# Optimization experiments

Measured on AMD Instinct MI355X. Metric: run time of the kernel, lower is better.

Reference implementation:

```python
import jax, jax.numpy as jnp
import numpy as np

K_PERIODS = 6


def setup_inputs() -> dict:
    key = jax.random.key(0)
    x = jax.random.normal(key, (16, 2048, 128), dtype=jnp.float32)
    return {"x": x}


def reference(x):
    # x: [B, T, N] -> out: [B, K, Pmax, N].
    # Pmax is data-dependent in the torch original (max selected period); here we
    # use the static upper bound Pmax = T so shapes are jit-static. Columns
    # p >= P_row are zero, matching the original's zero padding.
    B, T, N = x.shape
    BN = B * N
    seqs = jnp.transpose(x, (0, 2, 1)).reshape(BN, T)  # [BN, T]

    # --- top-k nonzero frequencies by spectral energy ---
    spec = jnp.fft.rfft(seqs, axis=-1)
    mag2 = spec.real ** 2 + spec.imag ** 2
    mag2 = mag2.at[:, 0].set(0.0)  # kill DC bin
    k = min(K_PERIODS, mag2.shape[-1] - 1)
    _, kidx = jax.lax.top_k(mag2, k)          # [BN, K]
    kidx = jnp.maximum(kidx, 1)

    # --- per-(row, freq) period geometry ---
    P = jnp.maximum(T // kidx, 1)             # [BN, K] period length
    cycles = jnp.maximum(T // P, 1)           # [BN, K] number of full cycles
    take = cycles * P
    base = jnp.maximum(T - take, 0)           # [BN, K] start offset

    # --- fold-and-average via scatter-add (no [BN,K,Cmax,Pmax] blowup) ---
    # element at time t >= base maps to phase p = (t - base) % P, averaged over cycles
    t = jnp.arange(T, dtype=jnp.int32)
    rel = t[None, None, :] - base[:, :, None]          # [BN, K, T]
    valid = rel >= 0
    p = jnp.where(valid, rel % P[:, :, None], 0)       # phase index in [0, P)
    vals = jnp.where(valid, seqs[:, None, :], 0.0)     # [BN, K, T]

    row = jnp.arange(BN * k, dtype=jnp.int32).reshape(BN, k, 1)
    seg_ids = row * T + p                               # flat segment id
    sums = jax.ops.segment_sum(vals.reshape(-1), seg_ids.reshape(-1),
                               num_segments=BN * k * T)
    seg = sums.reshape(BN, k, T) / cycles[:, :, None].astype(vals.dtype)

    out = seg.reshape(B, N, k, T).transpose(0, 2, 3, 1)  # [B, K, Pmax=T, N]
    return out
```

## Files before the change

### kernel.cpp

```cpp
#include <hip/hip_runtime.h>
#include <stdint.h>

#define TB   256
#define TLEN 2048
#define NB   16
#define NCH  128
#define BN   (NB*NCH)
#define KP   6

typedef unsigned long long u64;

__global__ __launch_bounds__(256) void k_fill0(float4* __restrict__ out, int n4) {
  int i = blockIdx.x * blockDim.x + threadIdx.x;
  int stride = gridDim.x * blockDim.x;
  float4 z = make_float4(0.f, 0.f, 0.f, 0.f);
  for (; i < n4; i += stride) out[i] = z;
}

__global__ __launch_bounds__(256) void k_transpose_in(const float* __restrict__ x,
                                                      float* __restrict__ seqs) {
  __shared__ float tile[64][65];
  int t0 = blockIdx.x * 64, n0 = blockIdx.y * 64, b = blockIdx.z;
  int tx = threadIdx.x & 63, ty = threadIdx.x >> 6;
#pragma unroll
  for (int tt = ty; tt < 64; tt += 4)
    tile[tt][tx] = x[(size_t)(b * TLEN + t0 + tt) * NCH + n0 + tx];
  __syncthreads();
#pragma unroll
  for (int nn = ty; nn < 64; nn += 4)
    seqs[(size_t)(b * NCH + n0 + nn) * TLEN + t0 + tx] = tile[tx][nn];
}

#define FT 512
__global__ __launch_bounds__(FT) void k_fft_topk(const float* __restrict__ seqs,
                                                 int4* __restrict__ params) {
  __shared__ float2 bufA[2048];
  __shared__ float2 bufB[2048];
  __shared__ float2 tw[1024];
  __shared__ u64 wmax[FT / 64];
  int tid = threadIdx.x;
  int r0 = blockIdx.x * 2;

  for (int t = tid; t < TLEN; t += FT) {
    float vr = seqs[(size_t)r0 * TLEN + t];
    float vi = seqs[(size_t)(r0 + 1) * TLEN + t];
    bufA[t] = make_float2(vr, vi);
  }
  const float c0 = -6.283185307179586f / 2048.0f;
  for (int j = tid; j < 1024; j += FT) {
    float sn, cs;
    sincosf(c0 * (float)j, &sn, &cs);
    tw[j] = make_float2(cs, sn);
  }

  float2* xb = bufA;
  float2* yb = bufB;
  for (int st = 0; st < 11; st++) {
    __syncthreads();
    int s = 1 << st;
#pragma unroll
    for (int ii = 0; ii < 1024 / FT; ii++) {
      int i = tid + ii * FT;
      int q = i & (s - 1);
      int p = i >> st;
      float2 a = xb[i];
      float2 b = xb[i + 1024];
      float2 w = tw[p << st];
      int o = q + (p << (st + 1));
      yb[o] = make_float2(a.x + b.x, a.y + b.y);
      float dx = a.x - b.x, dy = a.y - b.y;
      yb[o + s] = make_float2(dx * w.x - dy * w.y, dx * w.y + dy * w.x);
    }
    float2* t2 = xb; xb = yb; yb = t2;
  }
  __syncthreads();
  const float2* Z = xb;
  u64* keys = (u64*)bufA;
  for (int i = tid; i < 1024; i += FT) {
    int kb = i + 1;
    float2 zk = Z[kb];
    float2 zc = Z[2048 - kb];
    float ax = zk.x + zc.x, ay = zk.y - zc.y;
    float bx = zk.x - zc.x, by = zk.y + zc.y;
    float m2a = ax * ax + ay * ay;
    float m2b = bx * bx + by * by;
    keys[i]        = ((u64)__float_as_uint(m2a) << 32) | (unsigned)(0xFFFFFFFFu - (unsigned)kb);
    keys[1024 + i] = ((u64)__float_as_uint(m2b) << 32) | (unsigned)(0xFFFFFFFFu - (unsigned)kb);
  }
  __syncthreads();

  for (int rw = 0; rw < 2; rw++) {
    u64* kbase = keys + rw * 1024;
    for (int r = 0; r < KP; r++) {
      u64 best = 0ull;
      for (int i = tid; i < 1024; i += FT) {
        u64 v = kbase[i];
        best = v > best ? v : best;
      }
      for (int off = 32; off > 0; off >>= 1) {
        u64 o = __shfl_down(best, off);
        best = o > best ? o : best;
      }
      if ((tid & 63) == 0) wmax[tid >> 6] = best;
      __syncthreads();
      if (tid == 0) {
        best = wmax[0];
        for (int w = 1; w < FT / 64; w++) best = wmax[w] > best ? wmax[w] : best;
        int bin = (int)(0xFFFFFFFFu - (unsigned)(best & 0xFFFFFFFFull));
        if (bin < 1 || bin > 1024) bin = 1;
        kbase[bin - 1] = 0ull;
        int P = TLEN / bin;
        int cyc = TLEN / P;
        int base = TLEN - cyc * P;
        params[(r0 + rw) * KP + r] = make_int4(P, base, cyc, 0);
      }
      __syncthreads();
    }
  }
}

__global__ __launch_bounds__(256) void k_fold_row(const float* __restrict__ seqs,
                                                  const int4* __restrict__ params,
                                                  float* __restrict__ out) {
  __shared__ float srow[TLEN];
  __shared__ float acc[64];
  int row = blockIdx.x;
  int b = row >> 7, n = row & 127;
  int tid = threadIdx.x, lane = tid & 63, wv = tid >> 6;

  const float4* s4 = (const float4*)(seqs + (size_t)row * TLEN);
  float4* r4 = (float4*)srow;
  for (int i = tid; i < TLEN / 4; i += TB) r4[i] = s4[i];
  __syncthreads();

  for (int k = 0; k < KP; k++) {
    int4 pr = params[row * KP + k];
    int P = pr.x, base = pr.y, cyc = pr.z;
    float inv = 1.0f / (float)cyc;
    float* dst = out + (size_t)(b * KP + k) * TLEN * NCH + n;

    if (P >= 64) {
      for (int p0 = 0; p0 < P; p0 += TB) {
        int p = p0 + tid;
        if (p < P) {
          const float* sp = srow + base + p;
          float s = 0.f;
          for (int c = 0; c < cyc; c++) s += sp[c * P];
          dst[(size_t)p * NCH] = s * inv;
        }
      }
    } else {
      int wc = 64 / P;
      int u = wc * P;
      int ci = lane / P;
      int pi = lane - ci * P;
      float v = 0.f;
      if (lane < u) {
        for (int c0 = wv * wc; c0 < cyc; c0 += 4 * wc) {
          int c = c0 + ci;
          if (c < cyc) v += srow[base + c0 * P + lane];
        }
      }
      for (int s = P; s < u; s <<= 1) {
        float o = __shfl_down(v, s);
        if (lane + s < u) v += o;
      }
      if (tid < 64) acc[tid] = 0.f;
      __syncthreads();
      if (lane < P) atomicAdd(&acc[pi], v);
      __syncthreads();
      if (tid < P) dst[(size_t)tid * NCH] = acc[tid] * inv;
      __syncthreads();
    }
  }
}

extern "C" void kernel_launch(void* const* d_in, const int* in_sizes, int n_in,
                              void* d_out, int out_size, void* d_ws, size_t ws_size,
                              hipStream_t stream) {
  const float* x = (const float*)d_in[0];
  float* out = (float*)d_out;
  char* ws = (char*)d_ws;

  const size_t seqs_bytes = (size_t)BN * TLEN * 4;
  float* seqs = (float*)ws;
  int4* params = (int4*)(ws + seqs_bytes);

  k_fill0<<<8192, 256, 0, stream>>>((float4*)out, out_size / 4);
  k_transpose_in<<<dim3(TLEN / 64, NCH / 64, NB), 256, 0, stream>>>(x, seqs);
  k_fft_topk<<<dim3(BN / 2), FT, 0, stream>>>(seqs, params);
  k_fold_row<<<dim3(BN), 256, 0, stream>>>(seqs, params, out);
}
```

Baseline: 178.6 us.

## Use radix-4 FFT stages with padded LDS, parallel top-k, per-wave fold

Replaces the 11 radix-2 Stockham stages with five radix-4 stages plus a final radix-2 stage. Shared-memory indices are padded to avoid bank conflicts, and the FFT kernel drops from 512 to 256 threads. Top-k selection now runs for both packed rows in parallel on separate wave pairs, and the fold kernel assigns each period to its own wavefront, which removes the block-wide syncs and LDS atomics. The aim is fewer barriers and LDS passes in the FFT and less serialisation in the fold. In exchange, the FFT has fewer threads per block, and in the fold only two of four waves get a second period (6 periods over 4 waves), which may leave load imbalance.

```diff
diff --git a/kernel.cpp b/kernel.cpp
--- a/kernel.cpp
+++ b/kernel.cpp
@@ -10,6 +10,10 @@
 
 typedef unsigned long long u64;
 
+__device__ inline float2 cmul(float2 a, float2 b) {
+  return make_float2(a.x * b.x - a.y * b.y, a.x * b.y + a.y * b.x);
+}
+
 __global__ __launch_bounds__(256) void k_fill0(float4* __restrict__ out, int n4) {
   int i = blockIdx.x * blockDim.x + threadIdx.x;
   int stride = gridDim.x * blockDim.x;
@@ -31,23 +35,24 @@
     seqs[(size_t)(b * NCH + n0 + nn) * TLEN + t0 + tx] = tile[tx][nn];
 }
 
-#define FT 512
-__global__ __launch_bounds__(FT) void k_fft_topk(const float* __restrict__ seqs,
-                                                 int4* __restrict__ params) {
-  __shared__ float2 bufA[2048];
-  __shared__ float2 bufB[2048];
-  __shared__ float2 tw[1024];
-  __shared__ u64 wmax[FT / 64];
+#define PAD(o) ((o) + ((o) >> 4))
+__global__ __launch_bounds__(256) void k_fft_topk(const float* __restrict__ seqs,
+                                                  int4* __restrict__ params) {
+  __shared__ float2 bufA[2176];
+  __shared__ float2 bufB[2176];
+  __shared__ float2 tw[512];
+  __shared__ u64 wmax[4];
   int tid = threadIdx.x;
+  int lane = tid & 63, wv = tid >> 6;
   int r0 = blockIdx.x * 2;
 
-  for (int t = tid; t < TLEN; t += FT) {
+  for (int t = tid; t < TLEN; t += TB) {
     float vr = seqs[(size_t)r0 * TLEN + t];
     float vi = seqs[(size_t)(r0 + 1) * TLEN + t];
-    bufA[t] = make_float2(vr, vi);
+    bufA[PAD(t)] = make_float2(vr, vi);
   }
   const float c0 = -6.283185307179586f / 2048.0f;
-  for (int j = tid; j < 1024; j += FT) {
+  for (int j = tid; j < 512; j += TB) {
     float sn, cs;
     sincosf(c0 * (float)j, &sn, &cs);
     tw[j] = make_float2(cs, sn);
@@ -55,31 +60,54 @@
 
   float2* xb = bufA;
   float2* yb = bufB;
-  for (int st = 0; st < 11; st++) {
+#pragma unroll 1
+  for (int st2 = 0; st2 < 10; st2 += 2) {
+    int s = 1 << st2;
     __syncthreads();
-    int s = 1 << st;
-#pragma unroll
-    for (int ii = 0; ii < 1024 / FT; ii++) {
-      int i = tid + ii * FT;
+#pragma unroll
+    for (int ii = 0; ii < 2; ii++) {
+      int i = tid + ii * TB;
       int q = i & (s - 1);
-      int p = i >> st;
-      float2 a = xb[i];
-      float2 b = xb[i + 1024];
-      float2 w = tw[p << st];
-      int o = q + (p << (st + 1));
-      yb[o] = make_float2(a.x + b.x, a.y + b.y);
-      float dx = a.x - b.x, dy = a.y - b.y;
-      yb[o + s] = make_float2(dx * w.x - dy * w.y, dx * w.y + dy * w.x);
+      int cb = i - q;
+      float2 A0 = xb[PAD(i)];
+      float2 A1 = xb[PAD(i + 512)];
+      float2 A2 = xb[PAD(i + 1024)];
+      float2 A3 = xb[PAD(i + 1536)];
+      float2 S02 = make_float2(A0.x + A2.x, A0.y + A2.y);
+      float2 D02 = make_float2(A0.x - A2.x, A0.y - A2.y);
+      float2 S13 = make_float2(A1.x + A3.x, A1.y + A3.y);
+      float2 D13 = make_float2(A1.x - A3.x, A1.y - A3.y);
+      float2 b0 = make_float2(S02.x + S13.x, S02.y + S13.y);
+      float2 b1 = make_float2(D02.x + D13.y, D02.y - D13.x);
+      float2 b2 = make_float2(S02.x - S13.x, S02.y - S13.y);
+      float2 b3 = make_float2(D02.x - D13.y, D02.y + D13.x);
+      float2 w1 = tw[cb];
+      float2 w2 = make_float2(w1.x * w1.x - w1.y * w1.y, 2.f * w1.x * w1.y);
+      float2 w3 = cmul(w1, w2);
+      int o = q + 4 * cb;
+      yb[PAD(o)]         = b0;
+      yb[PAD(o + s)]     = cmul(w1, b1);
+      yb[PAD(o + 2 * s)] = cmul(w2, b2);
+      yb[PAD(o + 3 * s)] = cmul(w3, b3);
     }
     float2* t2 = xb; xb = yb; yb = t2;
   }
   __syncthreads();
-  const float2* Z = xb;
-  u64* keys = (u64*)bufA;
-  for (int i = tid; i < 1024; i += FT) {
+#pragma unroll
+  for (int ii = 0; ii < 4; ii++) {
+    int i = tid + ii * TB;
+    float2 a = xb[PAD(i)];
+    float2 b = xb[PAD(i + 1024)];
+    yb[PAD(i)]        = make_float2(a.x + b.x, a.y + b.y);
+    yb[PAD(i + 1024)] = make_float2(a.x - b.x, a.y - b.y);
+  }
+  __syncthreads();
+  const float2* Z = bufA;
+  u64* keys = (u64*)bufB;
+  for (int i = tid; i < 1024; i += TB) {
     int kb = i + 1;
-    float2 zk = Z[kb];
-    float2 zc = Z[2048 - kb];
+    float2 zk = Z[PAD(kb)];
+    float2 zc = Z[PAD(2048 - kb)];
     float ax = zk.x + zc.x, ay = zk.y - zc.y;
     float bx = zk.x - zc.x, by = zk.y + zc.y;
     float m2a = ax * ax + ay * ay;
@@ -89,33 +117,33 @@
   }
   __syncthreads();
 
-  for (int rw = 0; rw < 2; rw++) {
-    u64* kbase = keys + rw * 1024;
-    for (int r = 0; r < KP; r++) {
-      u64 best = 0ull;
-      for (int i = tid; i < 1024; i += FT) {
-        u64 v = kbase[i];
-        best = v > best ? v : best;
-      }
-      for (int off = 32; off > 0; off >>= 1) {
-        u64 o = __shfl_down(best, off);
-        best = o > best ? o : best;
-      }
-      if ((tid & 63) == 0) wmax[tid >> 6] = best;
-      __syncthreads();
-      if (tid == 0) {
-        best = wmax[0];
-        for (int w = 1; w < FT / 64; w++) best = wmax[w] > best ? wmax[w] : best;
-        int bin = (int)(0xFFFFFFFFu - (unsigned)(best & 0xFFFFFFFFull));
-        if (bin < 1 || bin > 1024) bin = 1;
-        kbase[bin - 1] = 0ull;
-        int P = TLEN / bin;
-        int cyc = TLEN / P;
-        int base = TLEN - cyc * P;
-        params[(r0 + rw) * KP + r] = make_int4(P, base, cyc, 0);
-      }
-      __syncthreads();
-    }
+  int rw = wv >> 1;
+  u64* kb2 = keys + rw * 1024;
+  int t2 = tid & 127;
+  for (int r = 0; r < KP; r++) {
+    u64 best = 0ull;
+    for (int i = t2; i < 1024; i += 128) {
+      u64 v = kb2[i];
+      best = v > best ? v : best;
+    }
+    for (int off = 32; off > 0; off >>= 1) {
+      u64 o = __shfl_down(best, off);
+      best = o > best ? o : best;
+    }
+    if (lane == 0) wmax[wv] = best;
+    __syncthreads();
+    if ((tid & 127) == 0) {
+      u64 b0 = wmax[rw * 2], b1 = wmax[rw * 2 + 1];
+      best = b0 > b1 ? b0 : b1;
+      int bin = (int)(0xFFFFFFFFu - (unsigned)(best & 0xFFFFFFFFull));
+      if (bin < 1 || bin > 1024) bin = 1;
+      kb2[bin - 1] = 0ull;
+      int P = TLEN / bin;
+      int cyc = TLEN / P;
+      int base = TLEN - cyc * P;
+      params[(r0 + rw) * KP + r] = make_int4(P, base, cyc, 0);
+    }
+    __syncthreads();
   }
 }
 
@@ -123,7 +151,6 @@
                                                   const int4* __restrict__ params,
                                                   float* __restrict__ out) {
   __shared__ float srow[TLEN];
-  __shared__ float acc[64];
   int row = blockIdx.x;
   int b = row >> 7, n = row & 127;
   int tid = threadIdx.x, lane = tid & 63, wv = tid >> 6;
@@ -133,30 +160,26 @@
   for (int i = tid; i < TLEN / 4; i += TB) r4[i] = s4[i];
   __syncthreads();
 
-  for (int k = 0; k < KP; k++) {
+  for (int k = wv; k < KP; k += 4) {
     int4 pr = params[row * KP + k];
     int P = pr.x, base = pr.y, cyc = pr.z;
     float inv = 1.0f / (float)cyc;
     float* dst = out + (size_t)(b * KP + k) * TLEN * NCH + n;
 
     if (P >= 64) {
-      for (int p0 = 0; p0 < P; p0 += TB) {
-        int p = p0 + tid;
-        if (p < P) {
-          const float* sp = srow + base + p;
-          float s = 0.f;
-          for (int c = 0; c < cyc; c++) s += sp[c * P];
-          dst[(size_t)p * NCH] = s * inv;
-        }
+      for (int p = lane; p < P; p += 64) {
+        const float* sp = srow + base + p;
+        float s = 0.f;
+        for (int c = 0; c < cyc; c++) s += sp[c * P];
+        dst[(size_t)p * NCH] = s * inv;
       }
     } else {
       int wc = 64 / P;
       int u = wc * P;
       int ci = lane / P;
-      int pi = lane - ci * P;
       float v = 0.f;
       if (lane < u) {
-        for (int c0 = wv * wc; c0 < cyc; c0 += 4 * wc) {
+        for (int c0 = 0; c0 < cyc; c0 += wc) {
           int c = c0 + ci;
           if (c < cyc) v += srow[base + c0 * P + lane];
         }
@@ -165,12 +188,7 @@
         float o = __shfl_down(v, s);
         if (lane + s < u) v += o;
       }
-      if (tid < 64) acc[tid] = 0.f;
-      __syncthreads();
-      if (lane < P) atomicAdd(&acc[pi], v);
-      __syncthreads();
-      if (tid < P) dst[(size_t)tid * NCH] = acc[tid] * inv;
-      __syncthreads();
+      if (lane < P) dst[(size_t)lane * NCH] = v * inv;
     }
   }
 }
@@ -188,6 +206,6 @@
 
   k_fill0<<<8192, 256, 0, stream>>>((float4*)out, out_size / 4);
   k_transpose_in<<<dim3(TLEN / 64, NCH / 64, NB), 256, 0, stream>>>(x, seqs);
-  k_fft_topk<<<dim3(BN / 2), FT, 0, stream>>>(seqs, params);
+  k_fft_topk<<<dim3(BN / 2), 256, 0, stream>>>(seqs, params);
   k_fold_row<<<dim3(BN), 256, 0, stream>>>(seqs, params, out);
 }
```

Result: faster. 154.3 us (-13.6%).
